# Optimization experiments

Hardware: AMD Instinct MI355X
Metric: run time of the kernel (lower is better)

The kernel has to match this reference:

```python
import jax, jax.numpy as jnp
import numpy as np

N_ZONE, E_ZONE = 100000, 2000000
N_OUT, E_OUT = 50000, 1000000
N_GND, E_GND = 50000, 1000000
HID = 64


def _gcn_conv(x, W, b, edge_index, edge_weight, num_nodes):
    """PyG GCNConv with normalize=True, add_self_loops=True (fill_value=1).
    out[i] = sum_{e: col[e]=i} d^-1/2[row]*w_e*d^-1/2[col] * (xW)[row[e]]
             + d^-1[i]*(xW)[i] + b
    """
    row, col = edge_index[0], edge_index[1]
    ew = edge_weight.reshape(-1)  # [E,1] -> [E]
    # degree includes self-loop weight of 1
    deg = jax.ops.segment_sum(ew, col, num_segments=num_nodes) + 1.0
    dinv = jnp.where(deg > 0, jax.lax.rsqrt(deg), 0.0)
    norm = dinv[row] * ew * dinv[col]  # [E]
    h = x @ W  # [N, HID] transform first (tiny in-dim)
    agg = jax.ops.segment_sum(norm[:, None] * h[row], col, num_segments=num_nodes)
    agg = agg + (dinv * dinv)[:, None] * h  # self-loop term
    return agg + b


def setup_inputs() -> dict:
    key = jax.random.key(0)
    ks = jax.random.split(key, 16)
    inp = {}
    inp["x_zone"] = jax.random.normal(ks[0], (N_ZONE, 2), dtype=jnp.float32)
    inp["x_outdoor"] = jax.random.normal(ks[1], (N_OUT, 3), dtype=jnp.float32)
    inp["x_ground"] = jax.random.normal(ks[2], (N_GND, 1), dtype=jnp.float32)
    inp["edge_index_zone"] = jax.random.randint(ks[3], (2, E_ZONE), 0, N_ZONE, dtype=jnp.int32)
    inp["edge_index_outdoor"] = jax.random.randint(ks[4], (2, E_OUT), 0, N_OUT, dtype=jnp.int32)
    inp["edge_index_ground"] = jax.random.randint(ks[5], (2, E_GND), 0, N_GND, dtype=jnp.int32)
    # learned params: GCN weights/biases + per-edge attribute parameters
    inp["W_zone"] = jax.random.normal(ks[6], (2, HID), dtype=jnp.float32) * 0.5
    inp["W_outdoor"] = jax.random.normal(ks[7], (3, HID), dtype=jnp.float32) * 0.5
    inp["W_ground"] = jax.random.normal(ks[8], (1, HID), dtype=jnp.float32) * 0.5
    inp["b_zone"] = jnp.zeros((HID,), dtype=jnp.float32)
    inp["b_outdoor"] = jnp.zeros((HID,), dtype=jnp.float32)
    inp["b_ground"] = jnp.zeros((HID,), dtype=jnp.float32)
    # positive edge weights so symmetric normalization deg^-1/2 is finite
    inp["edge_attr_zone"] = jax.random.uniform(ks[9], (E_ZONE, 1), dtype=jnp.float32, minval=0.1, maxval=1.0)
    inp["edge_attr_outdoor"] = jax.random.uniform(ks[10], (E_OUT, 1), dtype=jnp.float32, minval=0.1, maxval=1.0)
    inp["edge_attr_ground"] = jax.random.uniform(ks[11], (E_GND, 1), dtype=jnp.float32, minval=0.1, maxval=1.0)
    return inp


def reference(x_zone, x_outdoor, x_ground,
              edge_index_zone, edge_index_outdoor, edge_index_ground,
              W_zone, W_outdoor, W_ground,
              b_zone, b_outdoor, b_ground,
              edge_attr_zone, edge_attr_outdoor, edge_attr_ground):
    z = _gcn_conv(x_zone, W_zone, b_zone, edge_index_zone, edge_attr_zone, N_ZONE)
    o = _gcn_conv(x_outdoor, W_outdoor, b_outdoor, edge_index_outdoor, edge_attr_outdoor, N_OUT)
    g = _gcn_conv(x_ground, W_ground, b_ground, edge_index_ground, edge_attr_ground, N_GND)
    return (jax.nn.relu(z), jax.nn.relu(o), jax.nn.relu(g))
```

## Files before the change

### kernel.cpp

```cpp
#include <hip/hip_runtime.h>

#define N_ZONE 100000
#define E_ZONE 2000000
#define N_OUT  50000
#define E_OUT  1000000
#define N_GND  50000
#define E_GND  1000000
#define HID    64
#define N_TOT   (N_ZONE + N_OUT + N_GND)
#define E_TOTAL (E_ZONE + E_OUT + E_GND)

#define RANGE   2048
#define RSHIFT  11
#define NBZ     49
#define NBO     25
#define NBG     25
#define NBUCKET (NBZ + NBO + NBG)
#define SL      16
#define CAP     49152
#define OUT_PAD_BASE (NBZ * RANGE)
#define GND_PAD_BASE ((NBZ + NBO) * RANGE)
#define PAD_TOT      (NBUCKET * RANGE)

#define CHUNK  4096
#define NCHUNK ((E_TOTAL + CHUNK - 1) / CHUNK)

#define WCUR  0
#define WREC  128
#define WPDEG (WREC + 2 * NBUCKET * CAP)
#define WPSZ  (WPDEG + NBUCKET * SL * RANGE)
#define WPSO  (WPSZ + NBZ * SL * RANGE * 2)
#define WPSG  (WPSO + NBO * SL * RANGE * 3)
#define WDINV (WPSG + NBG * SL * RANGE)
#define WYZ   (WDINV + PAD_TOT)
#define WYO   (WYZ + 2 * N_ZONE)
#define WYG   (WYO + 4 * N_OUT)
#define WUZ   (WYG + N_GND)
#define WUO   (WUZ + 2 * N_ZONE)
#define WUG   (WUO + 4 * N_OUT)
#define WTOT  (WUG + N_GND)
#define FAST_WS_BYTES ((size_t)WTOT * 4)

__global__ void k_bin(const int* __restrict__ eiz, const float* __restrict__ wz,
                      const int* __restrict__ eio, const float* __restrict__ wo,
                      const int* __restrict__ eig, const float* __restrict__ wg,
                      unsigned* __restrict__ cur, uint2* __restrict__ rec) {
    __shared__ unsigned la[CHUNK];
    __shared__ float    lw[CHUNK];
    __shared__ unsigned hist[NBUCKET];
    __shared__ unsigned sbase[NBUCKET + 1];
    __shared__ unsigned gbase[NBUCKET];
    int tid = threadIdx.x;
    for (int b = tid; b < NBUCKET; b += 256) hist[b] = 0;
    __syncthreads();
    int t0 = blockIdx.x * CHUNK;
    unsigned mya[CHUNK / 256], mybk[CHUNK / 256], myr[CHUNK / 256];
    float myw[CHUNK / 256];
#pragma unroll
    for (int i = 0; i < CHUNK / 256; i++) {
        int t = t0 + i * 256 + tid;
        unsigned b = 0xFFFFFFFFu;
        if (t < E_TOTAL) {
            int row, col; float w;
            if (t < E_ZONE) { row = eiz[t]; col = eiz[E_ZONE + t]; w = wz[t]; b = col >> RSHIFT; }
            else if (t < E_ZONE + E_OUT) { int e = t - E_ZONE; row = eio[e]; col = eio[E_OUT + e]; w = wo[e]; b = NBZ + (col >> RSHIFT); }
            else { int e = t - E_ZONE - E_OUT; row = eig[e]; col = eig[E_GND + e]; w = wg[e]; b = NBZ + NBO + (col >> RSHIFT); }
            mya[i] = ((unsigned)(col & (RANGE - 1)) << 17) | (unsigned)row;
            myw[i] = w;
            myr[i] = atomicAdd(&hist[b], 1u);
        }
        mybk[i] = b;
    }
    __syncthreads();
    if (tid == 0) {
        unsigned acc = 0;
        for (int b = 0; b < NBUCKET; b++) { sbase[b] = acc; acc += hist[b]; }
        sbase[NBUCKET] = acc;
    }
    __syncthreads();
    if (tid < NBUCKET)
        gbase[tid] = hist[tid] ? atomicAdd(&cur[tid], hist[tid]) : 0u;
#pragma unroll
    for (int i = 0; i < CHUNK / 256; i++) {
        if (mybk[i] < NBUCKET) {
            unsigned p = sbase[mybk[i]] + myr[i];
            la[p] = mya[i]; lw[p] = myw[i];
        }
    }
    __syncthreads();
    unsigned total = sbase[NBUCKET];
    for (unsigned p = tid; p < total; p += 256) {
        int lo = 0, hi = NBUCKET;
        while (hi - lo > 1) { int mid = (lo + hi) >> 1; if (sbase[mid] <= p) lo = mid; else hi = mid; }
        unsigned idx = (unsigned)lo * CAP + gbase[lo] + (p - sbase[lo]);
        rec[idx] = make_uint2(la[p], __float_as_uint(lw[p]));
    }
}

__global__ void k_degp(const uint2* __restrict__ rec, const unsigned* __restrict__ cur,
                       float* __restrict__ pdeg) {
    __shared__ float deg[RANGE];
    int r = blockIdx.x / SL, sl = blockIdx.x % SL, tid = threadIdx.x;
    for (int i = tid; i < RANGE; i += 256) deg[i] = 0.0f;
    __syncthreads();
    unsigned c = cur[r];
    size_t b0 = (size_t)r * CAP;
    unsigned per = (c + SL - 1) / SL;
    unsigned s0 = sl * per, s1 = s0 + per; if (s1 > c) s1 = c;
    for (unsigned j = s0 + tid; j < s1; j += 256) {
        uint2 q = rec[b0 + j];
        atomicAdd(&deg[q.x >> 17], __uint_as_float(q.y));
    }
    __syncthreads();
    float* o = pdeg + (size_t)blockIdx.x * RANGE;
    for (int i = tid * 4; i < RANGE; i += 1024)
        *(float4*)&o[i] = *(float4*)&deg[i];
}

__global__ void k_dinvy(const float* __restrict__ xz, const float* __restrict__ xo,
                        const float* __restrict__ xg, float* __restrict__ ws) {
    int p = blockIdx.x * blockDim.x + threadIdx.x;
    if (p >= PAD_TOT) return;
    int r = p >> RSHIFT, i = p & (RANGE - 1);
    float d = 1.0f;
#pragma unroll
    for (int sl = 0; sl < SL; sl++)
        d += ws[WPDEG + (size_t)(r * SL + sl) * RANGE + i];
    float di = rsqrtf(d);
    ws[WDINV + p] = di;
    if (p < OUT_PAD_BASE) {
        if (p < N_ZONE) {
            ws[WYZ + 2 * p]     = di * xz[2 * p];
            ws[WYZ + 2 * p + 1] = di * xz[2 * p + 1];
        }
    } else if (p < GND_PAD_BASE) {
        int idx = p - OUT_PAD_BASE;
        if (idx < N_OUT) {
            ws[WYO + 4 * idx]     = di * xo[3 * idx];
            ws[WYO + 4 * idx + 1] = di * xo[3 * idx + 1];
            ws[WYO + 4 * idx + 2] = di * xo[3 * idx + 2];
            ws[WYO + 4 * idx + 3] = 0.0f;
        }
    } else {
        int idx = p - GND_PAD_BASE;
        if (idx < N_GND) ws[WYG + idx] = di * xg[idx];
    }
}

__global__ void k_sp(float* __restrict__ ws) {
    __shared__ __align__(16) float s[RANGE * 3];
    int r = blockIdx.x / SL, sl = blockIdx.x % SL, tid = threadIdx.x;
    const unsigned* cur = (const unsigned*)(ws + WCUR);
    const uint2* rec = (const uint2*)(ws + WREC);
    int ch, rg; size_t yoff, psoff;
    if (r < NBZ)            { ch = 2; rg = r;             yoff = WYZ; psoff = WPSZ; }
    else if (r < NBZ + NBO) { ch = 3; rg = r - NBZ;       yoff = WYO; psoff = WPSO; }
    else                    { ch = 1; rg = r - NBZ - NBO; yoff = WYG; psoff = WPSG; }
    int tot = RANGE * ch;
    for (int i = tid; i < tot; i += 256) s[i] = 0.0f;
    __syncthreads();
    unsigned c = cur[r];
    size_t b0 = (size_t)r * CAP;
    unsigned per = (c + SL - 1) / SL;
    unsigned s0 = sl * per, s1 = s0 + per; if (s1 > c) s1 = c;
    if (ch == 2) {
        const float2* y = (const float2*)(ws + yoff);
        for (unsigned j = s0 + tid; j < s1; j += 256) {
            uint2 q = rec[b0 + j];
            unsigned colr = q.x >> 17, row = q.x & 0x1FFFFu;
            float w = __uint_as_float(q.y);
            float2 yv = y[row];
            atomicAdd(&s[colr * 2],     w * yv.x);
            atomicAdd(&s[colr * 2 + 1], w * yv.y);
        }
    } else if (ch == 3) {
        const float4* y = (const float4*)(ws + yoff);
        for (unsigned j = s0 + tid; j < s1; j += 256) {
            uint2 q = rec[b0 + j];
            unsigned colr = q.x >> 17, row = q.x & 0x1FFFFu;
            float w = __uint_as_float(q.y);
            float4 yv = y[row];
            atomicAdd(&s[colr * 3],     w * yv.x);
            atomicAdd(&s[colr * 3 + 1], w * yv.y);
            atomicAdd(&s[colr * 3 + 2], w * yv.z);
        }
    } else {
        const float* y = ws + yoff;
        for (unsigned j = s0 + tid; j < s1; j += 256) {
            uint2 q = rec[b0 + j];
            atomicAdd(&s[q.x >> 17], __uint_as_float(q.y) * y[q.x & 0x1FFFFu]);
        }
    }
    __syncthreads();
    float* o = ws + psoff + (size_t)(rg * SL + sl) * tot;
    for (int i = tid * 4; i < tot; i += 1024)
        *(float4*)&o[i] = *(float4*)&s[i];
}

__global__ void k_u(float* __restrict__ ws) {
    int p = blockIdx.x * blockDim.x + threadIdx.x;
    if (p >= PAD_TOT) return;
    int r = p >> RSHIFT, i = p & (RANGE - 1);
    float di = ws[WDINV + p];
    if (p < OUT_PAD_BASE) {
        if (p >= N_ZONE) return;
        float s0 = ws[WYZ + 2 * p], s1 = ws[WYZ + 2 * p + 1];
#pragma unroll
        for (int sl = 0; sl < SL; sl++) {
            const float* ps = ws + WPSZ + (size_t)(r * SL + sl) * RANGE * 2;
            s0 += ps[2 * i]; s1 += ps[2 * i + 1];
        }
        ws[WUZ + 2 * p] = di * s0; ws[WUZ + 2 * p + 1] = di * s1;
    } else if (p < GND_PAD_BASE) {
        int idx = p - OUT_PAD_BASE;
        if (idx >= N_OUT) return;
        int rg = r - NBZ;
        float s0 = ws[WYO + 4 * idx], s1 = ws[WYO + 4 * idx + 1], s2 = ws[WYO + 4 * idx + 2];
#pragma unroll
        for (int sl = 0; sl < SL; sl++) {
            const float* ps = ws + WPSO + (size_t)(rg * SL + sl) * RANGE * 3;
            s0 += ps[3 * i]; s1 += ps[3 * i + 1]; s2 += ps[3 * i + 2];
        }
        ws[WUO + 4 * idx] = di * s0; ws[WUO + 4 * idx + 1] = di * s1; ws[WUO + 4 * idx + 2] = di * s2;
    } else {
        int idx = p - GND_PAD_BASE;
        if (idx >= N_GND) return;
        int rg = r - NBZ - NBO;
        float s0 = ws[WYG + idx];
#pragma unroll
        for (int sl = 0; sl < SL; sl++)
            s0 += ws[WPSG + (size_t)(rg * SL + sl) * RANGE + i];
        ws[WUG + idx] = di * s0;
    }
}

__global__ void k_fin2(const float* __restrict__ ws,
                       const float* __restrict__ Wz, const float* __restrict__ bz,
                       const float* __restrict__ Wo, const float* __restrict__ bo,
                       const float* __restrict__ Wg, const float* __restrict__ bg,
                       float* __restrict__ out) {
    int t = blockIdx.x * blockDim.x + threadIdx.x;
    const int TZ4 = N_ZONE * 16, TO4 = TZ4 + N_OUT * 16, TG4 = TO4 + N_GND * 16;
    if (t < TZ4) {
        int i = t >> 4, jb = (t & 15) << 2;
        float u0 = ws[WUZ + 2 * i], u1 = ws[WUZ + 2 * i + 1];
        float4 w0 = *(const float4*)(Wz + jb);
        float4 w1 = *(const float4*)(Wz + HID + jb);
        float4 bv = *(const float4*)(bz + jb);
        float4 o;
        o.x = fmaxf(bv.x + u0 * w0.x + u1 * w1.x, 0.0f);
        o.y = fmaxf(bv.y + u0 * w0.y + u1 * w1.y, 0.0f);
        o.z = fmaxf(bv.z + u0 * w0.z + u1 * w1.z, 0.0f);
        o.w = fmaxf(bv.w + u0 * w0.w + u1 * w1.w, 0.0f);
        *(float4*)(out + i * HID + jb) = o;
    } else if (t < TO4) {
        int q = t - TZ4;
        int i = q >> 4, jb = (q & 15) << 2;
        const float* u = ws + WUO + 4 * i;
        float u0 = u[0], u1 = u[1], u2 = u[2];
        float4 w0 = *(const float4*)(Wo + jb);
        float4 w1 = *(const float4*)(Wo + HID + jb);
        float4 w2 = *(const float4*)(Wo + 2 * HID + jb);
        float4 bv = *(const float4*)(bo + jb);
        float4 o;
        o.x = fmaxf(bv.x + u0 * w0.x + u1 * w1.x + u2 * w2.x, 0.0f);
        o.y = fmaxf(bv.y + u0 * w0.y + u1 * w1.y + u2 * w2.y, 0.0f);
        o.z = fmaxf(bv.z + u0 * w0.z + u1 * w1.z + u2 * w2.z, 0.0f);
        o.w = fmaxf(bv.w + u0 * w0.w + u1 * w1.w + u2 * w2.w, 0.0f);
        *(float4*)(out + N_ZONE * HID + i * HID + jb) = o;
    } else if (t < TG4) {
        int q = t - TO4;
        int i = q >> 4, jb = (q & 15) << 2;
        float u0 = ws[WUG + i];
        float4 w0 = *(const float4*)(Wg + jb);
        float4 bv = *(const float4*)(bg + jb);
        float4 o;
        o.x = fmaxf(bv.x + u0 * w0.x, 0.0f);
        o.y = fmaxf(bv.y + u0 * w0.y, 0.0f);
        o.z = fmaxf(bv.z + u0 * w0.z, 0.0f);
        o.w = fmaxf(bv.w + u0 * w0.w, 0.0f);
        *(float4*)(out + (N_ZONE + N_OUT) * HID + i * HID + jb) = o;
    }
}

#define F_DEG_Z   0
#define F_DEG_O   (N_ZONE)
#define F_DEG_G   (N_ZONE + N_OUT)
#define F_DEG_TOT N_TOT
#define F_S_Z     F_DEG_TOT
#define F_S_O     (F_S_Z + N_ZONE * 2)
#define F_S_G     (F_S_O + N_OUT * 3)
#define F_TOT     (F_S_G + N_GND * 1)

__global__ void f_init(float* __restrict__ ws) {
    int i = blockIdx.x * blockDim.x + threadIdx.x;
    if (i < F_TOT) ws[i] = (i < F_DEG_TOT) ? 1.0f : 0.0f;
}
__global__ void f_deg(const int* __restrict__ eiz, const float* __restrict__ wz,
                      const int* __restrict__ eio, const float* __restrict__ wo,
                      const int* __restrict__ eig, const float* __restrict__ wg,
                      float* __restrict__ ws) {
    int t = blockIdx.x * blockDim.x + threadIdx.x;
    if (t < E_ZONE) atomicAdd(ws + F_DEG_Z + eiz[E_ZONE + t], wz[t]);
    else if (t < E_ZONE + E_OUT) { int e = t - E_ZONE; atomicAdd(ws + F_DEG_O + eio[E_OUT + e], wo[e]); }
    else if (t < E_ZONE + E_OUT + E_GND) { int e = t - E_ZONE - E_OUT; atomicAdd(ws + F_DEG_G + eig[E_GND + e], wg[e]); }
}
__global__ void f_dinv(float* __restrict__ ws) {
    int i = blockIdx.x * blockDim.x + threadIdx.x;
    if (i < F_DEG_TOT) ws[i] = 1.0f / sqrtf(ws[i]);
}
__global__ void f_scatter(const int* __restrict__ eiz, const float* __restrict__ wz, const float* __restrict__ xz,
                          const int* __restrict__ eio, const float* __restrict__ wo, const float* __restrict__ xo,
                          const int* __restrict__ eig, const float* __restrict__ wg, const float* __restrict__ xg,
                          float* __restrict__ ws) {
    int t = blockIdx.x * blockDim.x + threadIdx.x;
    if (t < E_ZONE) {
        int row = eiz[t], col = eiz[E_ZONE + t];
        float n = ws[F_DEG_Z + row] * wz[t] * ws[F_DEG_Z + col];
        atomicAdd(ws + F_S_Z + col * 2 + 0, n * xz[row * 2 + 0]);
        atomicAdd(ws + F_S_Z + col * 2 + 1, n * xz[row * 2 + 1]);
    } else if (t < E_ZONE + E_OUT) {
        int e = t - E_ZONE;
        int row = eio[e], col = eio[E_OUT + e];
        float n = ws[F_DEG_O + row] * wo[e] * ws[F_DEG_O + col];
        atomicAdd(ws + F_S_O + col * 3 + 0, n * xo[row * 3 + 0]);
        atomicAdd(ws + F_S_O + col * 3 + 1, n * xo[row * 3 + 1]);
        atomicAdd(ws + F_S_O + col * 3 + 2, n * xo[row * 3 + 2]);
    } else if (t < E_ZONE + E_OUT + E_GND) {
        int e = t - E_ZONE - E_OUT;
        int row = eig[e], col = eig[E_GND + e];
        float n = ws[F_DEG_G + row] * wg[e] * ws[F_DEG_G + col];
        atomicAdd(ws + F_S_G + col, n * xg[row]);
    }
}
__global__ void f_final(const float* __restrict__ ws,
                        const float* __restrict__ xz, const float* __restrict__ Wz, const float* __restrict__ bz,
                        const float* __restrict__ xo, const float* __restrict__ Wo, const float* __restrict__ bo,
                        const float* __restrict__ xg, const float* __restrict__ Wg, const float* __restrict__ bg,
                        float* __restrict__ out) {
    int t = blockIdx.x * blockDim.x + threadIdx.x;
    const int TZ = N_ZONE * HID, TO = TZ + N_OUT * HID, TG = TO + N_GND * HID;
    if (t < TZ) {
        int i = t >> 6, j = t & 63;
        float di = ws[F_DEG_Z + i], d2 = di * di;
        float t0 = ws[F_S_Z + i * 2 + 0] + d2 * xz[i * 2 + 0];
        float t1 = ws[F_S_Z + i * 2 + 1] + d2 * xz[i * 2 + 1];
        out[t] = fmaxf(bz[j] + t0 * Wz[j] + t1 * Wz[HID + j], 0.0f);
    } else if (t < TO) {
        int u = t - TZ;
        int i = u >> 6, j = u & 63;
        float di = ws[F_DEG_O + i], d2 = di * di;
        float t0 = ws[F_S_O + i * 3 + 0] + d2 * xo[i * 3 + 0];
        float t1 = ws[F_S_O + i * 3 + 1] + d2 * xo[i * 3 + 1];
        float t2 = ws[F_S_O + i * 3 + 2] + d2 * xo[i * 3 + 2];
        out[t] = fmaxf(bo[j] + t0 * Wo[j] + t1 * Wo[HID + j] + t2 * Wo[2 * HID + j], 0.0f);
    } else if (t < TG) {
        int u = t - TO;
        int i = u >> 6, j = u & 63;
        float di = ws[F_DEG_G + i], d2 = di * di;
        float t0 = ws[F_S_G + i] + d2 * xg[i];
        out[t] = fmaxf(bg[j] + t0 * Wg[j], 0.0f);
    }
}

extern "C" void kernel_launch(void* const* d_in, const int* in_sizes, int n_in,
                              void* d_out, int out_size, void* d_ws, size_t ws_size,
                              hipStream_t stream) {
    const float* xz = (const float*)d_in[0];
    const float* xo = (const float*)d_in[1];
    const float* xg = (const float*)d_in[2];
    const int*  eiz = (const int*)d_in[3];
    const int*  eio = (const int*)d_in[4];
    const int*  eig = (const int*)d_in[5];
    const float* Wz = (const float*)d_in[6];
    const float* Wo = (const float*)d_in[7];
    const float* Wg = (const float*)d_in[8];
    const float* bz = (const float*)d_in[9];
    const float* bo = (const float*)d_in[10];
    const float* bg = (const float*)d_in[11];
    const float* wz = (const float*)d_in[12];
    const float* wo = (const float*)d_in[13];
    const float* wg = (const float*)d_in[14];
    float* out = (float*)d_out;
    float* ws  = (float*)d_ws;

    const int B = 256;

    if (ws_size >= FAST_WS_BYTES) {
        unsigned* cur = (unsigned*)(ws + WCUR);
        uint2* rec = (uint2*)(ws + WREC);
        hipMemsetAsync(cur, 0, 128 * 4, stream);
        k_bin<<<NCHUNK, B, 0, stream>>>(eiz, wz, eio, wo, eig, wg, cur, rec);
        k_degp<<<NBUCKET * SL, B, 0, stream>>>(rec, cur, ws + WPDEG);
        k_dinvy<<<(PAD_TOT + B - 1) / B, B, 0, stream>>>(xz, xo, xg, ws);
        k_sp<<<NBUCKET * SL, B, 0, stream>>>(ws);
        k_u<<<(PAD_TOT + B - 1) / B, B, 0, stream>>>(ws);
        k_fin2<<<(N_TOT * HID / 4 + B - 1) / B, B, 0, stream>>>(ws, Wz, bz, Wo, bo, Wg, bg, out);
    } else {
        const int E_TOT = E_TOTAL, OUT_TOT = N_TOT * HID;
        f_init<<<(F_TOT + B - 1) / B, B, 0, stream>>>(ws);
        f_deg<<<(E_TOT + B - 1) / B, B, 0, stream>>>(eiz, wz, eio, wo, eig, wg, ws);
        f_dinv<<<(F_DEG_TOT + B - 1) / B, B, 0, stream>>>(ws);
        f_scatter<<<(E_TOT + B - 1) / B, B, 0, stream>>>(eiz, wz, xz, eio, wo, xo, eig, wg, xg, ws);
        f_final<<<(OUT_TOT + B - 1) / B, B, 0, stream>>>(ws, xz, Wz, bz, xo, Wo, bo, xg, Wg, bg, out);
    }
}
```

Before: 248.3 us.

## Fuse partial-sum reduction into output kernel, unroll edge loops, drop bucket search

Merges the per-node partial-sum reduction kernel (k_u) into the final output kernel. Each block now reduces its nodes' partials into shared memory and then writes the 64-wide outputs, which removes one launch and the intermediate u buffer round trip. Edge loops in the degree and scatter kernels are unrolled by four so more independent gathers are in flight. The scatter kernel's slice count is halved, which shrinks the partial buffers at the cost of fewer blocks. The binning kernel also stores each edge's bucket id in shared memory instead of binary-searching for it.

Result: no change. 249.3 us (+0.4%).

```diff
diff --git a/kernel.cpp b/kernel.cpp
--- a/kernel.cpp
+++ b/kernel.cpp
@@ -16,7 +16,8 @@
 #define NBO     25
 #define NBG     25
 #define NBUCKET (NBZ + NBO + NBG)
-#define SL      16
+#define SL_D    16
+#define SL_S    8
 #define CAP     49152
 #define OUT_PAD_BASE (NBZ * RANGE)
 #define GND_PAD_BASE ((NBZ + NBO) * RANGE)
@@ -28,17 +29,14 @@
 #define WCUR  0
 #define WREC  128
 #define WPDEG (WREC + 2 * NBUCKET * CAP)
-#define WPSZ  (WPDEG + NBUCKET * SL * RANGE)
-#define WPSO  (WPSZ + NBZ * SL * RANGE * 2)
-#define WPSG  (WPSO + NBO * SL * RANGE * 3)
-#define WDINV (WPSG + NBG * SL * RANGE)
+#define WPSZ  (WPDEG + NBUCKET * SL_D * RANGE)
+#define WPSO  (WPSZ + NBZ * SL_S * RANGE * 2)
+#define WPSG  (WPSO + NBO * SL_S * RANGE * 3)
+#define WDINV (WPSG + NBG * SL_S * RANGE)
 #define WYZ   (WDINV + PAD_TOT)
 #define WYO   (WYZ + 2 * N_ZONE)
 #define WYG   (WYO + 4 * N_OUT)
-#define WUZ   (WYG + N_GND)
-#define WUO   (WUZ + 2 * N_ZONE)
-#define WUG   (WUO + 4 * N_OUT)
-#define WTOT  (WUG + N_GND)
+#define WTOT  (WYG + N_GND)
 #define FAST_WS_BYTES ((size_t)WTOT * 4)
 
 __global__ void k_bin(const int* __restrict__ eiz, const float* __restrict__ wz,
@@ -47,6 +45,7 @@
                       unsigned* __restrict__ cur, uint2* __restrict__ rec) {
     __shared__ unsigned la[CHUNK];
     __shared__ float    lw[CHUNK];
+    __shared__ unsigned char lbk[CHUNK];
     __shared__ unsigned hist[NBUCKET];
     __shared__ unsigned sbase[NBUCKET + 1];
     __shared__ unsigned gbase[NBUCKET];
@@ -84,14 +83,13 @@
     for (int i = 0; i < CHUNK / 256; i++) {
         if (mybk[i] < NBUCKET) {
             unsigned p = sbase[mybk[i]] + myr[i];
-            la[p] = mya[i]; lw[p] = myw[i];
+            la[p] = mya[i]; lw[p] = myw[i]; lbk[p] = (unsigned char)mybk[i];
         }
     }
     __syncthreads();
     unsigned total = sbase[NBUCKET];
     for (unsigned p = tid; p < total; p += 256) {
-        int lo = 0, hi = NBUCKET;
-        while (hi - lo > 1) { int mid = (lo + hi) >> 1; if (sbase[mid] <= p) lo = mid; else hi = mid; }
+        int lo = lbk[p];
         unsigned idx = (unsigned)lo * CAP + gbase[lo] + (p - sbase[lo]);
         rec[idx] = make_uint2(la[p], __float_as_uint(lw[p]));
     }
@@ -100,15 +98,23 @@
 __global__ void k_degp(const uint2* __restrict__ rec, const unsigned* __restrict__ cur,
                        float* __restrict__ pdeg) {
     __shared__ float deg[RANGE];
-    int r = blockIdx.x / SL, sl = blockIdx.x % SL, tid = threadIdx.x;
+    int r = blockIdx.x / SL_D, sl = blockIdx.x % SL_D, tid = threadIdx.x;
     for (int i = tid; i < RANGE; i += 256) deg[i] = 0.0f;
     __syncthreads();
     unsigned c = cur[r];
     size_t b0 = (size_t)r * CAP;
-    unsigned per = (c + SL - 1) / SL;
+    unsigned per = (((c + SL_D - 1) / SL_D) + 3) & ~3u;
     unsigned s0 = sl * per, s1 = s0 + per; if (s1 > c) s1 = c;
-    for (unsigned j = s0 + tid; j < s1; j += 256) {
-        uint2 q = rec[b0 + j];
+    unsigned jq = s1 & ~3u;
+    for (unsigned j = s0 + (tid << 2); j < jq; j += 1024) {
+        uint2 q0 = rec[b0 + j], q1 = rec[b0 + j + 1], q2 = rec[b0 + j + 2], q3 = rec[b0 + j + 3];
+        atomicAdd(&deg[q0.x >> 17], __uint_as_float(q0.y));
+        atomicAdd(&deg[q1.x >> 17], __uint_as_float(q1.y));
+        atomicAdd(&deg[q2.x >> 17], __uint_as_float(q2.y));
+        atomicAdd(&deg[q3.x >> 17], __uint_as_float(q3.y));
+    }
+    if (s0 <= jq && jq < s1 && tid < (int)(s1 - jq)) {
+        uint2 q = rec[b0 + jq + tid];
         atomicAdd(&deg[q.x >> 17], __uint_as_float(q.y));
     }
     __syncthreads();
@@ -124,8 +130,8 @@
     int r = p >> RSHIFT, i = p & (RANGE - 1);
     float d = 1.0f;
 #pragma unroll
-    for (int sl = 0; sl < SL; sl++)
-        d += ws[WPDEG + (size_t)(r * SL + sl) * RANGE + i];
+    for (int sl = 0; sl < SL_D; sl++)
+        d += ws[WPDEG + (size_t)(r * SL_D + sl) * RANGE + i];
     float di = rsqrtf(d);
     ws[WDINV + p] = di;
     if (p < OUT_PAD_BASE) {
@@ -149,7 +155,7 @@
 
 __global__ void k_sp(float* __restrict__ ws) {
     __shared__ __align__(16) float s[RANGE * 3];
-    int r = blockIdx.x / SL, sl = blockIdx.x % SL, tid = threadIdx.x;
+    int r = blockIdx.x / SL_S, sl = blockIdx.x % SL_S, tid = threadIdx.x;
     const unsigned* cur = (const unsigned*)(ws + WCUR);
     const uint2* rec = (const uint2*)(ws + WREC);
     int ch, rg; size_t yoff, psoff;
@@ -161,125 +167,180 @@
     __syncthreads();
     unsigned c = cur[r];
     size_t b0 = (size_t)r * CAP;
-    unsigned per = (c + SL - 1) / SL;
+    unsigned per = (((c + SL_S - 1) / SL_S) + 3) & ~3u;
     unsigned s0 = sl * per, s1 = s0 + per; if (s1 > c) s1 = c;
+    unsigned jq = s1 & ~3u;
     if (ch == 2) {
         const float2* y = (const float2*)(ws + yoff);
-        for (unsigned j = s0 + tid; j < s1; j += 256) {
-            uint2 q = rec[b0 + j];
-            unsigned colr = q.x >> 17, row = q.x & 0x1FFFFu;
+        for (unsigned j = s0 + (tid << 2); j < jq; j += 1024) {
+            uint2 q0 = rec[b0 + j], q1 = rec[b0 + j + 1], q2 = rec[b0 + j + 2], q3 = rec[b0 + j + 3];
+            float2 y0 = y[q0.x & 0x1FFFFu], y1 = y[q1.x & 0x1FFFFu];
+            float2 y2 = y[q2.x & 0x1FFFFu], y3 = y[q3.x & 0x1FFFFu];
+            float w0 = __uint_as_float(q0.y), w1 = __uint_as_float(q1.y);
+            float w2 = __uint_as_float(q2.y), w3 = __uint_as_float(q3.y);
+            atomicAdd(&s[(q0.x >> 17) * 2],     w0 * y0.x);
+            atomicAdd(&s[(q0.x >> 17) * 2 + 1], w0 * y0.y);
+            atomicAdd(&s[(q1.x >> 17) * 2],     w1 * y1.x);
+            atomicAdd(&s[(q1.x >> 17) * 2 + 1], w1 * y1.y);
+            atomicAdd(&s[(q2.x >> 17) * 2],     w2 * y2.x);
+            atomicAdd(&s[(q2.x >> 17) * 2 + 1], w2 * y2.y);
+            atomicAdd(&s[(q3.x >> 17) * 2],     w3 * y3.x);
+            atomicAdd(&s[(q3.x >> 17) * 2 + 1], w3 * y3.y);
+        }
+        if (s0 <= jq && jq < s1 && tid < (int)(s1 - jq)) {
+            uint2 q = rec[b0 + jq + tid];
+            float2 yv = y[q.x & 0x1FFFFu];
             float w = __uint_as_float(q.y);
-            float2 yv = y[row];
-            atomicAdd(&s[colr * 2],     w * yv.x);
-            atomicAdd(&s[colr * 2 + 1], w * yv.y);
+            atomicAdd(&s[(q.x >> 17) * 2],     w * yv.x);
+            atomicAdd(&s[(q.x >> 17) * 2 + 1], w * yv.y);
         }
     } else if (ch == 3) {
         const float4* y = (const float4*)(ws + yoff);
-        for (unsigned j = s0 + tid; j < s1; j += 256) {
-            uint2 q = rec[b0 + j];
-            unsigned colr = q.x >> 17, row = q.x & 0x1FFFFu;
+        for (unsigned j = s0 + (tid << 2); j < jq; j += 1024) {
+            uint2 q0 = rec[b0 + j], q1 = rec[b0 + j + 1], q2 = rec[b0 + j + 2], q3 = rec[b0 + j + 3];
+            float4 y0 = y[q0.x & 0x1FFFFu], y1 = y[q1.x & 0x1FFFFu];
+            float4 y2 = y[q2.x & 0x1FFFFu], y3 = y[q3.x & 0x1FFFFu];
+            float w0 = __uint_as_float(q0.y), w1 = __uint_as_float(q1.y);
+            float w2 = __uint_as_float(q2.y), w3 = __uint_as_float(q3.y);
+            unsigned c0 = (q0.x >> 17) * 3, c1 = (q1.x >> 17) * 3, c2 = (q2.x >> 17) * 3, c3 = (q3.x >> 17) * 3;
+            atomicAdd(&s[c0], w0 * y0.x); atomicAdd(&s[c0 + 1], w0 * y0.y); atomicAdd(&s[c0 + 2], w0 * y0.z);
+            atomicAdd(&s[c1], w1 * y1.x); atomicAdd(&s[c1 + 1], w1 * y1.y); atomicAdd(&s[c1 + 2], w1 * y1.z);
+            atomicAdd(&s[c2], w2 * y2.x); atomicAdd(&s[c2 + 1], w2 * y2.y); atomicAdd(&s[c2 + 2], w2 * y2.z);
+            atomicAdd(&s[c3], w3 * y3.x); atomicAdd(&s[c3 + 1], w3 * y3.y); atomicAdd(&s[c3 + 2], w3 * y3.z);
+        }
+        if (s0 <= jq && jq < s1 && tid < (int)(s1 - jq)) {
+            uint2 q = rec[b0 + jq + tid];
+            float4 yv = y[q.x & 0x1FFFFu];
             float w = __uint_as_float(q.y);
-            float4 yv = y[row];
-            atomicAdd(&s[colr * 3],     w * yv.x);
-            atomicAdd(&s[colr * 3 + 1], w * yv.y);
-            atomicAdd(&s[colr * 3 + 2], w * yv.z);
+            unsigned cc = (q.x >> 17) * 3;
+            atomicAdd(&s[cc], w * yv.x); atomicAdd(&s[cc + 1], w * yv.y); atomicAdd(&s[cc + 2], w * yv.z);
         }
     } else {
         const float* y = ws + yoff;
-        for (unsigned j = s0 + tid; j < s1; j += 256) {
-            uint2 q = rec[b0 + j];
+        for (unsigned j = s0 + (tid << 2); j < jq; j += 1024) {
+            uint2 q0 = rec[b0 + j], q1 = rec[b0 + j + 1], q2 = rec[b0 + j + 2], q3 = rec[b0 + j + 3];
+            float y0 = y[q0.x & 0x1FFFFu], y1 = y[q1.x & 0x1FFFFu];
+            float y2 = y[q2.x & 0x1FFFFu], y3 = y[q3.x & 0x1FFFFu];
+            atomicAdd(&s[q0.x >> 17], __uint_as_float(q0.y) * y0);
+            atomicAdd(&s[q1.x >> 17], __uint_as_float(q1.y) * y1);
+            atomicAdd(&s[q2.x >> 17], __uint_as_float(q2.y) * y2);
+            atomicAdd(&s[q3.x >> 17], __uint_as_float(q3.y) * y3);
+        }
+        if (s0 <= jq && jq < s1 && tid < (int)(s1 - jq)) {
+            uint2 q = rec[b0 + jq + tid];
             atomicAdd(&s[q.x >> 17], __uint_as_float(q.y) * y[q.x & 0x1FFFFu]);
         }
     }
     __syncthreads();
-    float* o = ws + psoff + (size_t)(rg * SL + sl) * tot;
+    float* o = ws + psoff + (size_t)(rg * SL_S + sl) * tot;
     for (int i = tid * 4; i < tot; i += 1024)
         *(float4*)&o[i] = *(float4*)&s[i];
 }
 
-__global__ void k_u(float* __restrict__ ws) {
-    int p = blockIdx.x * blockDim.x + threadIdx.x;
-    if (p >= PAD_TOT) return;
-    int r = p >> RSHIFT, i = p & (RANGE - 1);
-    float di = ws[WDINV + p];
-    if (p < OUT_PAD_BASE) {
-        if (p >= N_ZONE) return;
-        float s0 = ws[WYZ + 2 * p], s1 = ws[WYZ + 2 * p + 1];
-#pragma unroll
-        for (int sl = 0; sl < SL; sl++) {
-            const float* ps = ws + WPSZ + (size_t)(r * SL + sl) * RANGE * 2;
-            s0 += ps[2 * i]; s1 += ps[2 * i + 1];
-        }
-        ws[WUZ + 2 * p] = di * s0; ws[WUZ + 2 * p + 1] = di * s1;
-    } else if (p < GND_PAD_BASE) {
-        int idx = p - OUT_PAD_BASE;
-        if (idx >= N_OUT) return;
-        int rg = r - NBZ;
-        float s0 = ws[WYO + 4 * idx], s1 = ws[WYO + 4 * idx + 1], s2 = ws[WYO + 4 * idx + 2];
-#pragma unroll
-        for (int sl = 0; sl < SL; sl++) {
-            const float* ps = ws + WPSO + (size_t)(rg * SL + sl) * RANGE * 3;
-            s0 += ps[3 * i]; s1 += ps[3 * i + 1]; s2 += ps[3 * i + 2];
-        }
-        ws[WUO + 4 * idx] = di * s0; ws[WUO + 4 * idx + 1] = di * s1; ws[WUO + 4 * idx + 2] = di * s2;
-    } else {
-        int idx = p - GND_PAD_BASE;
-        if (idx >= N_GND) return;
-        int rg = r - NBZ - NBO;
-        float s0 = ws[WYG + idx];
-#pragma unroll
-        for (int sl = 0; sl < SL; sl++)
-            s0 += ws[WPSG + (size_t)(rg * SL + sl) * RANGE + i];
-        ws[WUG + idx] = di * s0;
-    }
-}
-
-__global__ void k_fin2(const float* __restrict__ ws,
+#define NBKZ ((N_ZONE + 127) / 128)
+#define NBKO ((N_OUT + 63) / 64)
+#define NBKG ((N_GND + 255) / 256)
+__global__ void k_fin3(const float* __restrict__ ws,
                        const float* __restrict__ Wz, const float* __restrict__ bz,
                        const float* __restrict__ Wo, const float* __restrict__ bo,
                        const float* __restrict__ Wg, const float* __restrict__ bg,
                        float* __restrict__ out) {
-    int t = blockIdx.x * blockDim.x + threadIdx.x;
-    const int TZ4 = N_ZONE * 16, TO4 = TZ4 + N_OUT * 16, TG4 = TO4 + N_GND * 16;
-    if (t < TZ4) {
-        int i = t >> 4, jb = (t & 15) << 2;
-        float u0 = ws[WUZ + 2 * i], u1 = ws[WUZ + 2 * i + 1];
-        float4 w0 = *(const float4*)(Wz + jb);
-        float4 w1 = *(const float4*)(Wz + HID + jb);
-        float4 bv = *(const float4*)(bz + jb);
-        float4 o;
-        o.x = fmaxf(bv.x + u0 * w0.x + u1 * w1.x, 0.0f);
-        o.y = fmaxf(bv.y + u0 * w0.y + u1 * w1.y, 0.0f);
-        o.z = fmaxf(bv.z + u0 * w0.z + u1 * w1.z, 0.0f);
-        o.w = fmaxf(bv.w + u0 * w0.w + u1 * w1.w, 0.0f);
-        *(float4*)(out + i * HID + jb) = o;
-    } else if (t < TO4) {
-        int q = t - TZ4;
-        int i = q >> 4, jb = (q & 15) << 2;
-        const float* u = ws + WUO + 4 * i;
-        float u0 = u[0], u1 = u[1], u2 = u[2];
-        float4 w0 = *(const float4*)(Wo + jb);
-        float4 w1 = *(const float4*)(Wo + HID + jb);
-        float4 w2 = *(const float4*)(Wo + 2 * HID + jb);
-        float4 bv = *(const float4*)(bo + jb);
-        float4 o;
-        o.x = fmaxf(bv.x + u0 * w0.x + u1 * w1.x + u2 * w2.x, 0.0f);
-        o.y = fmaxf(bv.y + u0 * w0.y + u1 * w1.y + u2 * w2.y, 0.0f);
-        o.z = fmaxf(bv.z + u0 * w0.z + u1 * w1.z + u2 * w2.z, 0.0f);
-        o.w = fmaxf(bv.w + u0 * w0.w + u1 * w1.w + u2 * w2.w, 0.0f);
-        *(float4*)(out + N_ZONE * HID + i * HID + jb) = o;
-    } else if (t < TG4) {
-        int q = t - TO4;
-        int i = q >> 4, jb = (q & 15) << 2;
-        float u0 = ws[WUG + i];
-        float4 w0 = *(const float4*)(Wg + jb);
-        float4 bv = *(const float4*)(bg + jb);
-        float4 o;
-        o.x = fmaxf(bv.x + u0 * w0.x, 0.0f);
-        o.y = fmaxf(bv.y + u0 * w0.y, 0.0f);
-        o.z = fmaxf(bv.z + u0 * w0.z, 0.0f);
-        o.w = fmaxf(bv.w + u0 * w0.w, 0.0f);
-        *(float4*)(out + (N_ZONE + N_OUT) * HID + i * HID + jb) = o;
+    __shared__ float su[256];
+    int bid = blockIdx.x, tid = threadIdx.x;
+    if (bid < NBKZ) {
+        int n0 = bid * 128;
+        int n = n0 + (tid >> 1), c = tid & 1;
+        if (n < N_ZONE) {
+            int r = n >> RSHIFT, i = n & (RANGE - 1);
+            float sum = ws[WYZ + 2 * n + c];
+#pragma unroll
+            for (int sl = 0; sl < SL_S; sl++)
+                sum += ws[WPSZ + (size_t)(r * SL_S + sl) * (RANGE * 2) + 2 * i + c];
+            su[tid] = ws[WDINV + n] * sum;
+        }
+        __syncthreads();
+#pragma unroll
+        for (int k = 0; k < 8; k++) {
+            int f = tid + k * 256;
+            int node = f >> 4, jb = (f & 15) << 2;
+            int n2 = n0 + node;
+            if (n2 < N_ZONE) {
+                float u0 = su[2 * node], u1 = su[2 * node + 1];
+                float4 w0 = *(const float4*)(Wz + jb);
+                float4 w1 = *(const float4*)(Wz + HID + jb);
+                float4 bv = *(const float4*)(bz + jb);
+                float4 o;
+                o.x = fmaxf(bv.x + u0 * w0.x + u1 * w1.x, 0.0f);
+                o.y = fmaxf(bv.y + u0 * w0.y + u1 * w1.y, 0.0f);
+                o.z = fmaxf(bv.z + u0 * w0.z + u1 * w1.z, 0.0f);
+                o.w = fmaxf(bv.w + u0 * w0.w + u1 * w1.w, 0.0f);
+                *(float4*)(out + (size_t)n2 * HID + jb) = o;
+            }
+        }
+    } else if (bid < NBKZ + NBKO) {
+        int n0 = (bid - NBKZ) * 64;
+        if (tid < 192) {
+            int n = n0 + tid / 3, c = tid % 3;
+            if (n < N_OUT) {
+                int p = OUT_PAD_BASE + n;
+                int rg = (p >> RSHIFT) - NBZ, i = p & (RANGE - 1);
+                float sum = ws[WYO + 4 * n + c];
+#pragma unroll
+                for (int sl = 0; sl < SL_S; sl++)
+                    sum += ws[WPSO + (size_t)(rg * SL_S + sl) * (RANGE * 3) + 3 * i + c];
+                su[tid] = ws[WDINV + p] * sum;
+            }
+        }
+        __syncthreads();
+#pragma unroll
+        for (int k = 0; k < 4; k++) {
+            int f = tid + k * 256;
+            int node = f >> 4, jb = (f & 15) << 2;
+            int n2 = n0 + node;
+            if (n2 < N_OUT) {
+                float u0 = su[3 * node], u1 = su[3 * node + 1], u2 = su[3 * node + 2];
+                float4 w0 = *(const float4*)(Wo + jb);
+                float4 w1 = *(const float4*)(Wo + HID + jb);
+                float4 w2 = *(const float4*)(Wo + 2 * HID + jb);
+                float4 bv = *(const float4*)(bo + jb);
+                float4 o;
+                o.x = fmaxf(bv.x + u0 * w0.x + u1 * w1.x + u2 * w2.x, 0.0f);
+                o.y = fmaxf(bv.y + u0 * w0.y + u1 * w1.y + u2 * w2.y, 0.0f);
+                o.z = fmaxf(bv.z + u0 * w0.z + u1 * w1.z + u2 * w2.z, 0.0f);
+                o.w = fmaxf(bv.w + u0 * w0.w + u1 * w1.w + u2 * w2.w, 0.0f);
+                *(float4*)(out + (size_t)(N_ZONE + n2) * HID + jb) = o;
+            }
+        }
+    } else {
+        int n0 = (bid - NBKZ - NBKO) * 256;
+        int n = n0 + tid;
+        if (n < N_GND) {
+            int p = GND_PAD_BASE + n;
+            int rg = (p >> RSHIFT) - NBZ - NBO, i = p & (RANGE - 1);
+            float sum = ws[WYG + n];
+#pragma unroll
+            for (int sl = 0; sl < SL_S; sl++)
+                sum += ws[WPSG + (size_t)(rg * SL_S + sl) * RANGE + i];
+            su[tid] = ws[WDINV + p] * sum;
+        }
+        __syncthreads();
+#pragma unroll
+        for (int k = 0; k < 16; k++) {
+            int f = tid + k * 256;
+            int node = f >> 4, jb = (f & 15) << 2;
+            int n2 = n0 + node;
+            if (n2 < N_GND) {
+                float u0 = su[node];
+                float4 w0 = *(const float4*)(Wg + jb);
+                float4 bv = *(const float4*)(bg + jb);
+                float4 o;
+                o.x = fmaxf(bv.x + u0 * w0.x, 0.0f);
+                o.y = fmaxf(bv.y + u0 * w0.y, 0.0f);
+                o.z = fmaxf(bv.z + u0 * w0.z, 0.0f);
+                o.w = fmaxf(bv.w + u0 * w0.w, 0.0f);
+                *(float4*)(out + (size_t)(N_ZONE + N_OUT + n2) * HID + jb) = o;
+            }
+        }
     }
 }
 
@@ -391,11 +452,10 @@
         uint2* rec = (uint2*)(ws + WREC);
         hipMemsetAsync(cur, 0, 128 * 4, stream);
         k_bin<<<NCHUNK, B, 0, stream>>>(eiz, wz, eio, wo, eig, wg, cur, rec);
-        k_degp<<<NBUCKET * SL, B, 0, stream>>>(rec, cur, ws + WPDEG);
+        k_degp<<<NBUCKET * SL_D, B, 0, stream>>>(rec, cur, ws + WPDEG);
         k_dinvy<<<(PAD_TOT + B - 1) / B, B, 0, stream>>>(xz, xo, xg, ws);
-        k_sp<<<NBUCKET * SL, B, 0, stream>>>(ws);
-        k_u<<<(PAD_TOT + B - 1) / B, B, 0, stream>>>(ws);
-        k_fin2<<<(N_TOT * HID / 4 + B - 1) / B, B, 0, stream>>>(ws, Wz, bz, Wo, bo, Wg, bg, out);
+        k_sp<<<NBUCKET * SL_S, B, 0, stream>>>(ws);
+        k_fin3<<<NBKZ + NBKO + NBKG, B, 0, stream>>>(ws, Wz, bz, Wo, bo, Wg, bg, out);
     } else {
         const int E_TOT = E_TOTAL, OUT_TOT = N_TOT * HID;
         f_init<<<(F_TOT + B - 1) / B, B, 0, stream>>>(ws);
```
